# Kernel optimization log

Hardware: AMD Instinct MI355X
Metric: run time of the kernel (lower is better)

## Reference

```python
import jax, jax.numpy as jnp
import numpy as np

PI = float(np.pi)
BN_EPS = 1e-3
LN_EPS = 1e-5


def ssslu(x, shape, bias):
    # x * (sin(softsign(x) * shape*pi/2) + (bias + 1))
    s = x / (1.0 + jnp.abs(x))
    return x * (jnp.sin(s * (shape * PI / 2.0)) + (bias + 1.0))


def bn(x, g, b, m, v):
    inv = (g / jnp.sqrt(v + BN_EPS))[None, :, None, None]
    return (x - m[None, :, None, None]) * inv + b[None, :, None, None]


def conv2d(x, w, bias=None, pad=0):
    y = jax.lax.conv_general_dilated(x, w, (1, 1), [(pad, pad), (pad, pad)],
                                     dimension_numbers=('NCHW', 'OIHW', 'NCHW'))
    if bias is not None:
        y = y + bias[None, :, None, None]
    return y


def ln_silu(v):
    # LayerNorm (unit weight, zero bias) over last axis, then SiLU
    mu = jnp.mean(v, axis=-1, keepdims=True)
    var = jnp.mean(jnp.square(v - mu), axis=-1, keepdims=True)
    h = (v - mu) / jnp.sqrt(var + LN_EPS)
    return h * jax.nn.sigmoid(h)


def _forward(x, w_qkv, g_qkv, b_qkv, m_qkv, v_qkv,
             w_co, g_co, b_co, m_co, v_co,
             w_b1, bias_b1, g_b1, b_b1, m_b1, v_b1,
             w_b2, bias_b2, g_b2, b_b2, m_b2, v_b2):
    B, C, H, W = x.shape
    Q = (w_qkv.shape[0] - C) // 2
    # qkv Conv block: conv1x1 -> SSSLU(-3, 0.3) -> BN
    t = bn(ssslu(conv2d(x, w_qkv, pad=0), -3.0, 0.3), g_qkv, b_qkv, m_qkv, v_qkv)
    xq, xk, xv = jnp.split(t, [Q, 2 * Q], axis=1)
    # max-pooled Q/K rows and columns -> [B*Q, W] / [B*Q, H]
    qw = jnp.max(xq, axis=2).reshape(B * Q, W)
    kw = jnp.max(xk, axis=2).reshape(B * Q, W)
    qh = jnp.max(xq, axis=3).reshape(B * Q, H)
    kh = jnp.max(xk, axis=3).reshape(B * Q, H)
    # xaw[i,b] = max_a qw[i,a]*kw[i,b]; xah[i,a] = max_b qh[i,a]*kh[i,b]
    xaw = jnp.max(qw[:, :, None] * kw[:, None, :], axis=1)  # [BQ, W]
    xah = jnp.max(qh[:, :, None] * kh[:, None, :], axis=2)  # [BQ, H]
    xaw = ln_silu(xaw)
    xah = ln_silu(xah)
    xa = (xah[:, :, None] * xaw[:, None, :]).reshape(B, Q, H, W)
    # co: SSSLUConv(Q+C -> Q): conv3x3 -> BN -> SSSLU(1.0, 0)
    xa = jnp.concatenate([xa, xv], axis=1)
    xa = ssslu(bn(conv2d(xa, w_co, pad=1), g_co, b_co, m_co, v_co), 1.0, 0.0)
    # back[0]: Conv(Q -> C, k3, bias): conv -> SSSLU(-3, 0.3) -> BN
    xa = bn(ssslu(conv2d(xa, w_b1, bias_b1, pad=1), -3.0, 0.3), g_b1, b_b1, m_b1, v_b1)
    # back[1]: SSSLUConv(C -> C, k1, bias): conv -> BN -> SSSLU(0.8, 0)
    xa = ssslu(bn(conv2d(xa, w_b2, bias_b2, pad=0), g_b2, b_b2, m_b2, v_b2), 0.8, 0.0)
    # back[2]: Sigmoid; source returns the gate itself
    return jax.nn.sigmoid(xa)


def setup_inputs() -> dict:
    B, C, Q, H, W = 16, 256, 256, 64, 64
    key = jax.random.key(0)
    ks = jax.random.split(key, 32)

    def w_init(k, o, i, kh, kw):
        return jax.random.normal(k, (o, i, kh, kw), jnp.float32) * (1.0 / np.sqrt(i * kh * kw))

    def bn_params(k, c):
        k1, k2, k3, k4 = jax.random.split(k, 4)
        g = jax.random.uniform(k1, (c,), jnp.float32, 0.5, 1.5)
        b = jax.random.normal(k2, (c,), jnp.float32) * 0.1
        m = jax.random.normal(k3, (c,), jnp.float32) * 0.1
        v = jax.random.uniform(k4, (c,), jnp.float32, 0.5, 1.5)
        return g, b, m, v

    x = jax.random.normal(ks[0], (B, C, H, W), jnp.float32)
    w_qkv = w_init(ks[1], 2 * Q + C, C, 1, 1)
    g_qkv, b_qkv, m_qkv, v_qkv = bn_params(ks[2], 2 * Q + C)
    w_co = w_init(ks[3], Q, Q + C, 3, 3)
    g_co, b_co, m_co, v_co = bn_params(ks[4], Q)
    w_b1 = w_init(ks[5], C, Q, 3, 3)
    bias_b1 = jax.random.normal(ks[6], (C,), jnp.float32) * 0.05
    g_b1, b_b1, m_b1, v_b1 = bn_params(ks[7], C)
    w_b2 = w_init(ks[8], C, C, 1, 1)
    bias_b2 = jax.random.normal(ks[9], (C,), jnp.float32) * 0.05
    g_b2, b_b2, m_b2, v_b2 = bn_params(ks[10], C)
    return dict(x=x, w_qkv=w_qkv, g_qkv=g_qkv, b_qkv=b_qkv, m_qkv=m_qkv, v_qkv=v_qkv,
                w_co=w_co, g_co=g_co, b_co=b_co, m_co=m_co, v_co=v_co,
                w_b1=w_b1, bias_b1=bias_b1, g_b1=g_b1, b_b1=b_b1, m_b1=m_b1, v_b1=v_b1,
                w_b2=w_b2, bias_b2=bias_b2, g_b2=g_b2, b_b2=b_b2, m_b2=m_b2, v_b2=v_b2)


def reference(x, w_qkv, g_qkv, b_qkv, m_qkv, v_qkv,
              w_co, g_co, b_co, m_co, v_co,
              w_b1, bias_b1, g_b1, b_b1, m_b1, v_b1,
              w_b2, bias_b2, g_b2, b_b2, m_b2, v_b2):
    return _forward(x, w_qkv, g_qkv, b_qkv, m_qkv, v_qkv,
                    w_co, g_co, b_co, m_co, v_co,
                    w_b1, bias_b1, g_b1, b_b1, m_b1, v_b1,
                    w_b2, bias_b2, g_b2, b_b2, m_b2, v_b2)
```

## Files before the change

kernel.cpp:

```cpp
#include <hip/hip_runtime.h>
#include <hip/hip_bf16.h>
#include <math.h>

#define PI_F 3.14159265358979323846f

typedef unsigned short u16;
typedef unsigned int   u32;
typedef float    f32x4 __attribute__((ext_vector_type(4)));
typedef _Float16 f16x8 __attribute__((ext_vector_type(8)));
typedef u16      u16x8 __attribute__((ext_vector_type(8)));
typedef u16      u16x4 __attribute__((ext_vector_type(4)));

__device__ __forceinline__ u16 f2h(float f){ union{ _Float16 h; u16 u; } c; c.h = (_Float16)f; return c.u; }
__device__ __forceinline__ float h2f(u16 u){ union{ u16 u; _Float16 h; } c; c.u = u; return (float)c.h; }

__device__ __forceinline__ void gl16(const void* g, void* l){
  __builtin_amdgcn_global_load_lds((const __attribute__((address_space(1))) u32*)g,
                                   (__attribute__((address_space(3))) u32*)l, 16, 0, 0);
}

__device__ __forceinline__ int SWZ(int r){ return (r>>1)&3; }

__device__ __forceinline__ float wred_max(float v){
#pragma unroll
  for (int m = 32; m; m >>= 1) v = fmaxf(v, __shfl_xor(v, m));
  return v;
}
__device__ __forceinline__ float wred_min(float v){
#pragma unroll
  for (int m = 32; m; m >>= 1) v = fminf(v, __shfl_xor(v, m));
  return v;
}
__device__ __forceinline__ float wred_sum(float v){
#pragma unroll
  for (int m = 32; m; m >>= 1) v += __shfl_xor(v, m);
  return v;
}

__device__ __forceinline__ float ssslu_f(float x, float shp, float bp1){
  float s = x / (1.0f + fabsf(x));
  return x * (__sinf(s * shp) + bp1);
}

__device__ __forceinline__ float epi_val(float v, float4 p, float shp, float bp1, int ORDER, bool SIG){
  v += p.w;
  if (ORDER == 0){ v = ssslu_f(v, shp, bp1); v = (v - p.z) * p.x + p.y; }
  else           { v = (v - p.z) * p.x + p.y; v = ssslu_f(v, shp, bp1); }
  if (SIG) v = 1.f / (1.f + __expf(-v));
  return v;
}

__device__ __forceinline__ void atomicMaxF(float* a, float v){
  if (v >= 0.f) atomicMax(reinterpret_cast<int*>(a), __float_as_int(v));
  else          atomicMin(reinterpret_cast<unsigned int*>(a), __float_as_uint(v));
}

__device__ __forceinline__ f16x8 mul8h(u16x8 a, u16x8 b){
  union{ u16x8 u; f16x8 h; } A, B; A.u = a; B.u = b;
  return A.h * B.h;
}

__global__ __launch_bounds__(256)
void xpose_k(const float* __restrict__ X, u16* __restrict__ XH)
{
  __shared__ u16 L[16384];
  const int tid = threadIdx.x;
  const int b = blockIdx.x >> 6, h = blockIdx.x & 63;
  const float* xp = X + (size_t)b * 256 * 4096 + h * 64;
#pragma unroll
  for (int i = 0; i < 16; ++i){
    int ci = i * 16 + (tid >> 4);
    int w4 = (tid & 15) * 4;
    float4 v = *(const float4*)(xp + (size_t)ci * 4096 + w4);
    int sw = 4 * ((ci >> 3) & 15);
    u16x4 d;
    d[0] = f2h(v.x); d[1] = f2h(v.y); d[2] = f2h(v.z); d[3] = f2h(v.w);
    *(u16x4*)&L[ci * 64 + (w4 ^ sw)] = d;
  }
  __syncthreads();
  u16* out = XH + (((size_t)b * 4096 + (size_t)h * 64) << 8);
#pragma unroll
  for (int it = 0; it < 8; ++it){
    int w   = it * 8 + (tid >> 5);
    int m   = tid & 31;
    int ci0 = m * 8;
    int base = (w & ~3) ^ (4 * (m & 15));
    int wl   = w & 3;
    u16x8 o;
#pragma unroll
    for (int k = 0; k < 8; ++k)
      o[k] = L[(ci0 + k) * 64 + base + wl];
    *(u16x8*)&out[w * 256 + ci0] = o;
  }
}

template<int CI_T, bool CAT>
__global__ __launch_bounds__(512, 2)
void conv3_mfma(const u16* __restrict__ Apk, const u16* __restrict__ Bg,
                u16* __restrict__ DstH, const float4* __restrict__ pp,
                const u16* __restrict__ xahT_, const u16* __restrict__ xawT_,
                float shp, float bp1, int ORDER)
{
  constexpr int NCC = CI_T / 32;
  constexpr int NIT = NCC * 3;
  __shared__ __align__(16) u16 sAB[73728];

  const int tid  = threadIdx.x;
  const int lane = tid & 63;
  const int wv   = tid >> 6;
  const int wm   = wv >> 2;
  const int wn   = wv & 3;
  const int l15  = lane & 15, l4 = lane >> 4;

  const int bx  = blockIdx.x;
  const int bid = (bx & 7) * 32 + (bx >> 3);
  const int b   = bid >> 4;
  const int r0  = (bid & 15) * 4;

  auto STAGE = [&](int it2){
    int d2 = it2 % 3, c2 = it2 / 3;
    if (d2 == 0){
      int bufB = c2 & 1;
#pragma unroll
      for (int j = 0; j < 3; ++j){
        int rr  = 2 * j + (tid >> 8);
        int hh  = r0 - 1 + rr; hh = min(63, max(0, hh));
        int rem = tid & 255;
        int w   = rem >> 2, s = rem & 3;
        int ci0 = c2 * 32 + ((s ^ SWZ(w + 1)) << 3);
        if (CAT && c2 < 8){
          u16x8 vh = *(const u16x8*)&xahT_[((b * 64 + hh) << 8) + ci0];
          u16x8 vw = *(const u16x8*)&xawT_[((b * 64 + w ) << 8) + ci0];
          *(f16x8*)&sAB[49152 + bufB * 12288 + rr * 2048 + w * 32 + s * 8] = mul8h(vh, vw);
        } else {
          int ci = CAT ? (ci0 - 256) : ci0;
          const u16* src = Bg + (((size_t)b * 4096 + hh * 64 + w) << 8) + ci;
          gl16(src, &sAB[49152 + bufB * 12288 + rr * 2048 + (wv & 3) * 512]);
        }
      }
    }
    int bufA = it2 & 1;
#pragma unroll
    for (int j2 = 0; j2 < 3; ++j2){
      int tap = d2 * 3 + j2;
      const u16* base = Apk + (size_t)tap * 256 * CI_T + c2 * 32;
#pragma unroll
      for (int i = 0; i < 2; ++i){
        int row = i * 128 + (tid >> 2);
        int s   = tid & 3;
        const u16* src = base + (size_t)row * CI_T + ((s ^ SWZ(row)) << 3);
        gl16(src, &sAB[bufA * 24576 + j2 * 8192 + (i * 128 + wv * 16) * 32]);
      }
    }
  };

  f32x4 acc[8][4];
#pragma unroll
  for (int i = 0; i < 8; ++i)
#pragma unroll
    for (int j = 0; j < 4; ++j){ acc[i][j][0]=0.f; acc[i][j][1]=0.f; acc[i][j][2]=0.f; acc[i][j][3]=0.f; }

  STAGE(0);
  __syncthreads();

  for (int it = 0; it < NIT; ++it){
    if (it + 1 < NIT) STAGE(it + 1);

    const int d = it % 3, c = it / 3;
    const int bufA = it & 1, bufB = c & 1;
    const int brow = wn + d;
    const bool rowok = ((unsigned)(r0 + wn + d - 1)) < 64u;

#pragma unroll
    for (int dw = 0; dw < 3; ++dw){
      f16x8 afr[8], bfr[4];
#pragma unroll
      for (int fm = 0; fm < 8; ++fm){
        int m  = wm * 128 + fm * 16 + l15;
        int sl = l4 ^ SWZ(m);
        afr[fm] = *(const f16x8*)&sAB[bufA * 24576 + dw * 8192 + m * 32 + sl * 8];
      }
#pragma unroll
      for (int fn = 0; fn < 4; ++fn){
        int w_in = fn * 16 + l15 + dw - 1;
        int wc   = min(63, max(0, w_in));
        int sl2  = l4 ^ SWZ(wc + 1);
        f16x8 t  = *(const f16x8*)&sAB[49152 + bufB * 12288 + brow * 2048 + wc * 32 + sl2 * 8];
        bool ok  = rowok && (((unsigned)w_in) < 64u);
        bfr[fn]  = ok ? t : (f16x8)(_Float16)0;
      }
      __builtin_amdgcn_s_setprio(1);
#pragma unroll
      for (int fm = 0; fm < 8; ++fm)
#pragma unroll
        for (int fn = 0; fn < 4; ++fn)
          acc[fm][fn] = __builtin_amdgcn_mfma_f32_16x16x32_f16(afr[fm], bfr[fn], acc[fm][fn], 0, 0, 0);
      __builtin_amdgcn_s_setprio(0);
    }
    __syncthreads();
  }

  const int h = r0 + wn;
#pragma unroll
  for (int fm = 0; fm < 8; ++fm){
    const int cobase = wm * 128 + fm * 16 + 4 * l4;
    float4 P0 = pp[cobase], P1 = pp[cobase+1], P2 = pp[cobase+2], P3 = pp[cobase+3];
#pragma unroll
    for (int fn = 0; fn < 4; ++fn){
      int w = fn * 16 + l15;
      float v0 = epi_val(acc[fm][fn][0], P0, shp, bp1, ORDER, false);
      float v1 = epi_val(acc[fm][fn][1], P1, shp, bp1, ORDER, false);
      float v2 = epi_val(acc[fm][fn][2], P2, shp, bp1, ORDER, false);
      float v3 = epi_val(acc[fm][fn][3], P3, shp, bp1, ORDER, false);
      uint2 st;
      st.x = (u32)f2h(v0) | ((u32)f2h(v1) << 16);
      st.y = (u32)f2h(v2) | ((u32)f2h(v3) << 16);
      *(uint2*)&DstH[(((size_t)b * 4096 + (size_t)h * 64 + w) << 8) + cobase] = st;
    }
  }
}

template<int SRC, int EPI, int HLOOP>
__global__ __launch_bounds__(256)
void conv_mfma(const u16* __restrict__ Apk, const u16* __restrict__ Bg,
               u16* __restrict__ DstH, float* __restrict__ DstF,
               const float4* __restrict__ pp,
               const float* __restrict__ Xf,
               float* __restrict__ qwp, float* __restrict__ kwp,
               float* __restrict__ qhp, float* __restrict__ khp,
               float shp, float bp1, int ORDER, int M)
{
  constexpr int NCC = 8;
  constexpr int HG  = 64 / HLOOP;
  __shared__ __align__(16) u16 sA[2][8192];
  __shared__ __align__(16) u16 sB[2][2112];

  const int tid  = threadIdx.x;
  const int lane = tid & 63;
  const int wv   = tid >> 6;
  const int bx   = blockIdx.x;
  const int b    = bx / HG;
  const int h0   = (bx % HG) * HLOOP;
  const int m0   = blockIdx.y * 256;

  f32x4 acc[4][4];
  f32x4 cmax[4][4];
  if (EPI == 0){
#pragma unroll
    for (int i = 0; i < 4; ++i)
#pragma unroll
      for (int j = 0; j < 4; ++j){ cmax[i][j][0]=-3.0e38f; cmax[i][j][1]=-3.0e38f; cmax[i][j][2]=-3.0e38f; cmax[i][j][3]=-3.0e38f; }
  }

  for (int hi = 0; hi < HLOOP; ++hi){
    const int h = h0 + hi;
#pragma unroll
    for (int i = 0; i < 4; ++i)
#pragma unroll
      for (int j = 0; j < 4; ++j){ acc[i][j][0]=0.f; acc[i][j][1]=0.f; acc[i][j][2]=0.f; acc[i][j][3]=0.f; }

    auto stageA = [&](int c, int buf){
      const u16* base = Apk + (size_t)m0 * 256 + c * 32;
#pragma unroll
      for (int i = 0; i < 4; ++i){
        int row = i * 64 + (tid >> 2);
        int s   = tid & 3;
        const u16* src = base + (size_t)row * 256 + ((s ^ SWZ(row)) << 3);
        gl16(src, &sA[buf][(i * 64 + wv * 16) * 32]);
      }
    };
    auto stageB = [&](int c, int buf){
      const int w = tid >> 2, s = tid & 3, r = w + 1;
      if (SRC == 0){
        int ci0 = c * 32 + ((s ^ SWZ(r)) << 3);
        const float* xp = Xf + ((size_t)(b * 256 + ci0)) * 4096 + h * 64 + w;
        u16x8 v;
#pragma unroll
        for (int j = 0; j < 8; ++j) v[j] = f2h(xp[(size_t)j * 4096]);
        *(u16x8*)&sB[buf][r * 32 + s * 8] = v;
      } else {
        const u16* src = Bg + (((size_t)b * 4096 + h * 64 + w) << 8) + c * 32 + ((s ^ SWZ(r)) << 3);
        gl16(src, &sB[buf][(1 + wv * 16) * 32]);
      }
    };

    __syncthreads();
    stageA(0, 0);
    stageB(0, 0);
    __syncthreads();

    for (int it = 0; it < NCC; ++it){
      if (it + 1 < NCC){ stageA(it + 1, (it + 1) & 1); stageB(it + 1, (it + 1) & 1); }
      f16x8 afr[4], bfr[4];
#pragma unroll
      for (int fm = 0; fm < 4; ++fm){
        int row = wv * 64 + fm * 16 + (lane & 15);
        int sl  = (lane >> 4) ^ SWZ(row);
        afr[fm] = *(const f16x8*)&sA[it & 1][row * 32 + sl * 8];
      }
#pragma unroll
      for (int fn = 0; fn < 4; ++fn){
        int r  = fn * 16 + (lane & 15) + 1;
        int sl = (lane >> 4) ^ SWZ(r);
        bfr[fn] = *(const f16x8*)&sB[it & 1][r * 32 + sl * 8];
      }
      __builtin_amdgcn_s_setprio(1);
#pragma unroll
      for (int fm = 0; fm < 4; ++fm)
#pragma unroll
        for (int fn = 0; fn < 4; ++fn)
          acc[fm][fn] = __builtin_amdgcn_mfma_f32_16x16x32_f16(afr[fm], bfr[fn], acc[fm][fn], 0, 0, 0);
      __builtin_amdgcn_s_setprio(0);
      __syncthreads();
    }

    const int l15 = lane & 15, l4 = lane >> 4;
    if (EPI == 0){
#pragma unroll
      for (int fm = 0; fm < 4; ++fm){
        const int cobase = m0 + wv * 64 + fm * 16 + 4 * l4;
        float4 P0 = pp[cobase], P1 = pp[cobase+1], P2 = pp[cobase+2], P3 = pp[cobase+3];
        f32x4 ev[4];
#pragma unroll
        for (int fn = 0; fn < 4; ++fn){
          ev[fn][0] = epi_val(acc[fm][fn][0], P0, shp, bp1, ORDER, false);
          ev[fn][1] = epi_val(acc[fm][fn][1], P1, shp, bp1, ORDER, false);
          ev[fn][2] = epi_val(acc[fm][fn][2], P2, shp, bp1, ORDER, false);
          ev[fn][3] = epi_val(acc[fm][fn][3], P3, shp, bp1, ORDER, false);
#pragma unroll
          for (int r = 0; r < 4; ++r) cmax[fm][fn][r] = fmaxf(cmax[fm][fn][r], ev[fn][r]);
        }
#pragma unroll
        for (int r = 0; r < 4; ++r){
          float mv = fmaxf(fmaxf(ev[0][r], ev[1][r]), fmaxf(ev[2][r], ev[3][r]));
          mv = fmaxf(mv, __shfl_xor(mv, 1));
          mv = fmaxf(mv, __shfl_xor(mv, 2));
          mv = fmaxf(mv, __shfl_xor(mv, 4));
          mv = fmaxf(mv, __shfl_xor(mv, 8));
          if (l15 == 0){
            int q = (cobase + r) & 255;
            float* rowp = (m0 == 0) ? qhp : khp;
            rowp[(((b << 8) | q) << 6) + h] = mv;
          }
        }
      }
    } else if (EPI == 1){
#pragma unroll
      for (int fm = 0; fm < 4; ++fm){
        const int cobase = wv * 64 + fm * 16 + 4 * l4;
        float4 P0 = pp[cobase], P1 = pp[cobase+1], P2 = pp[cobase+2], P3 = pp[cobase+3];
#pragma unroll
        for (int fn = 0; fn < 4; ++fn){
          int w = fn * 16 + l15;
          float v0 = epi_val(acc[fm][fn][0], P0, shp, bp1, ORDER, false);
          float v1 = epi_val(acc[fm][fn][1], P1, shp, bp1, ORDER, false);
          float v2 = epi_val(acc[fm][fn][2], P2, shp, bp1, ORDER, false);
          float v3 = epi_val(acc[fm][fn][3], P3, shp, bp1, ORDER, false);
          uint2 st;
          st.x = (u32)f2h(v0) | ((u32)f2h(v1) << 16);
          st.y = (u32)f2h(v2) | ((u32)f2h(v3) << 16);
          *(uint2*)&DstH[(((size_t)b * 4096 + (size_t)h * 64 + w) << 8) + cobase] = st;
        }
      }
    } else {
#pragma unroll
      for (int fm = 0; fm < 4; ++fm){
        const int cobase = wv * 64 + fm * 16 + 4 * l4;
        float4 P0 = pp[cobase], P1 = pp[cobase+1], P2 = pp[cobase+2], P3 = pp[cobase+3];
#pragma unroll
        for (int fn = 0; fn < 4; ++fn){
          int w = fn * 16 + l15;
          float v0 = epi_val(acc[fm][fn][0], P0, shp, bp1, ORDER, true);
          float v1 = epi_val(acc[fm][fn][1], P1, shp, bp1, ORDER, true);
          float v2 = epi_val(acc[fm][fn][2], P2, shp, bp1, ORDER, true);
          float v3 = epi_val(acc[fm][fn][3], P3, shp, bp1, ORDER, true);
          size_t base = ((size_t)(b * 256 + cobase)) * 4096 + h * 64 + w;
          DstF[base]          = v0;
          DstF[base + 4096]   = v1;
          DstF[base + 2*4096] = v2;
          DstF[base + 3*4096] = v3;
        }
      }
    }
  }

  if (EPI == 0){
    const int l15 = lane & 15, l4 = lane >> 4;
    float* colp = (m0 == 0) ? qwp : kwp;
#pragma unroll
    for (int fm = 0; fm < 4; ++fm)
#pragma unroll
      for (int fn = 0; fn < 4; ++fn)
#pragma unroll
        for (int r = 0; r < 4; ++r){
          int q = (m0 + wv * 64 + fm * 16 + 4 * l4 + r) & 255;
          int w = fn * 16 + l15;
          atomicMaxF(&colp[(((b << 8) | q) << 6) + w], cmax[fm][fn][r]);
        }
  }
}

__device__ __forceinline__ float ln_silu_wave(float v){
  float mu = wred_sum(v) * (1.f / 64.f);
  float d = v - mu;
  float var = wred_sum(d * d) * (1.f / 64.f);
  float hn = d * rsqrtf(var + 1e-5f);
  return hn / (1.f + __expf(-hn));
}

__global__ void attn_k(const float* __restrict__ qw, const float* __restrict__ kw,
                       const float* __restrict__ qh, const float* __restrict__ kh,
                       u16* __restrict__ xahT, u16* __restrict__ xawT)
{
  int row  = blockIdx.x * 4 + (threadIdx.x >> 6);
  int lane = threadIdx.x & 63;
  int idx  = (row << 6) + lane;
  float qwv = qw[idx], kwv = kw[idx], qhv = qh[idx], khv = kh[idx];
  float Pq = wred_max(qwv), mq = wred_min(qwv);
  float Pk = wred_max(khv), mk = wred_min(khv);
  float aw = fmaxf(kwv * Pq, kwv * mq);
  float ah = fmaxf(qhv * Pk, qhv * mk);
  aw = ln_silu_wave(aw);
  ah = ln_silu_wave(ah);
  int b = row >> 8, q = row & 255;
  xawT[((b * 64 + lane) << 8) + q] = f2h(aw);
  xahT[((b * 64 + lane) << 8) + q] = f2h(ah);
}

__global__ void pack_k(const float* __restrict__ wqkv, const float* __restrict__ wco,
                       const float* __restrict__ wb1, const float* __restrict__ wb2,
                       const float* gq, const float* bq, const float* mq, const float* vq,
                       const float* gc, const float* bc, const float* mc, const float* vc,
                       const float* g1, const float* b1, const float* m1, const float* v1, const float* bias1,
                       const float* g2, const float* b2, const float* m2, const float* v2, const float* bias2,
                       u16* __restrict__ WQ, u16* __restrict__ WCO, u16* __restrict__ WB1, u16* __restrict__ WB2,
                       float4* __restrict__ PP)
{
  const int E0 = 196608, E1 = 196608 + 1179648, E2 = 196608 + 1179648 + 589824, E3 = 2031616;
  int i = blockIdx.x * 256 + threadIdx.x;
  if (i >= E3 + 1536) return;
  if (i < E0){ WQ[i] = f2h(wqkv[i]); }
  else if (i < E1){
    int d = i - E0; int tap = d / 131072; int rm = d % 131072; int m = rm >> 9; int ci = rm & 511;
    WCO[d] = f2h(wco[(size_t)((m << 9) | ci) * 9 + tap]);
  } else if (i < E2){
    int d = i - E1; int tap = d / 65536; int rm = d & 65535; int m = rm >> 8; int ci = rm & 255;
    WB1[d] = f2h(wb1[(size_t)((m << 8) | ci) * 9 + tap]);
  } else if (i < E3){
    int d = i - E2; WB2[d] = f2h(wb2[d]);
  } else {
    int c = i - E3;
    float g, be, mm, vv, bi;
    if (c < 768){ g = gq[c]; be = bq[c]; mm = mq[c]; vv = vq[c]; bi = 0.f; }
    else if (c < 1024){ int j = c - 768;  g = gc[j]; be = bc[j]; mm = mc[j]; vv = vc[j]; bi = 0.f; }
    else if (c < 1280){ int j = c - 1024; g = g1[j]; be = b1[j]; mm = m1[j]; vv = v1[j]; bi = bias1[j]; }
    else              { int j = c - 1280; g = g2[j]; be = b2[j]; mm = m2[j]; vv = v2[j]; bi = bias2[j]; }
    PP[c] = make_float4(g / sqrtf(vv + 1e-3f), be, mm, bi);
  }
}

__global__ void initpool_k(float* __restrict__ p)
{
  int i = blockIdx.x * 1024 + threadIdx.x * 4;
  float4 v = make_float4(-3.0e38f, -3.0e38f, -3.0e38f, -3.0e38f);
  *(float4*)(p + i) = v;
}

extern "C" void kernel_launch(void* const* d_in, const int* in_sizes, int n_in,
                              void* d_out, int out_size, void* d_ws, size_t ws_size,
                              hipStream_t stream)
{
  const float* x       = (const float*)d_in[0];
  const float* w_qkv   = (const float*)d_in[1];
  const float* g_qkv   = (const float*)d_in[2];
  const float* b_qkv   = (const float*)d_in[3];
  const float* m_qkv   = (const float*)d_in[4];
  const float* v_qkv   = (const float*)d_in[5];
  const float* w_co    = (const float*)d_in[6];
  const float* g_co    = (const float*)d_in[7];
  const float* b_co    = (const float*)d_in[8];
  const float* m_co    = (const float*)d_in[9];
  const float* v_co    = (const float*)d_in[10];
  const float* w_b1    = (const float*)d_in[11];
  const float* bias_b1 = (const float*)d_in[12];
  const float* g_b1    = (const float*)d_in[13];
  const float* b_b1    = (const float*)d_in[14];
  const float* m_b1    = (const float*)d_in[15];
  const float* v_b1    = (const float*)d_in[16];
  const float* w_b2    = (const float*)d_in[17];
  const float* bias_b2 = (const float*)d_in[18];
  const float* g_b2    = (const float*)d_in[19];
  const float* b_b2    = (const float*)d_in[20];
  const float* m_b2    = (const float*)d_in[21];
  const float* v_b2    = (const float*)d_in[22];
  float* out = (float*)d_out;

  char* W = (char*)d_ws;
  u16*    WQ   = (u16*)(W + 0);
  u16*    WCO  = (u16*)(W + 393216);
  u16*    WB1  = (u16*)(W + 2752512);
  u16*    WB2  = (u16*)(W + 3932160);
  float4* PP   = (float4*)(W + 4063232);
  u16*    TV   = (u16*)(W + 4087808);
  u16*    XAHT = (u16*)(W + 37642240);
  u16*    XAWT = (u16*)(W + 38166528);
  u16*    XH   = (u16*)(W + 38690816);
  u16*    Y1   = (u16*)(W + 38690816);
  u16*    Y2   = TV;
  float*  qw_  = (float*)(W + 72245248);
  float*  kw_  = (float*)(W + 73293824);
  float*  qh_  = (float*)(W + 74342400);
  float*  kh_  = (float*)(W + 75390976);

  const size_t NEED = 76439552;
  if (ws_size < NEED) return;

  const float SHP_N3 = -3.0f * PI_F * 0.5f;
  const float SHP_1  =  1.0f * PI_F * 0.5f;
  const float SHP_08 =  0.8f * PI_F * 0.5f;

  dim3 blk(256);

  pack_k<<<7942, blk, 0, stream>>>(w_qkv, w_co, w_b1, w_b2,
      g_qkv, b_qkv, m_qkv, v_qkv,
      g_co,  b_co,  m_co,  v_co,
      g_b1,  b_b1,  m_b1,  v_b1,  bias_b1,
      g_b2,  b_b2,  m_b2,  v_b2,  bias_b2,
      WQ, WCO, WB1, WB2, PP);

  initpool_k<<<512, blk, 0, stream>>>(qw_);

  xpose_k<<<1024, blk, 0, stream>>>(x, XH);

  conv_mfma<1, 0, 4><<<dim3(256, 2), blk, 0, stream>>>(
      WQ, XH, nullptr, nullptr, PP, nullptr,
      qw_, kw_, qh_, kh_, SHP_N3, 1.3f, 0, 512);

  conv_mfma<1, 1, 1><<<dim3(1024, 1), blk, 0, stream>>>(
      WQ + (size_t)512 * 256, XH, TV, nullptr, PP + 512, nullptr,
      nullptr, nullptr, nullptr, nullptr, SHP_N3, 1.3f, 0, 256);

  attn_k<<<1024, blk, 0, stream>>>(qw_, kw_, qh_, kh_, XAHT, XAWT);

  conv3_mfma<512, true><<<256, 512, 0, stream>>>(
      WCO, TV, Y1, PP + 768, XAHT, XAWT, SHP_1, 1.0f, 1);

  conv3_mfma<256, false><<<256, 512, 0, stream>>>(
      WB1, Y1, Y2, PP + 1024, nullptr, nullptr, SHP_N3, 1.3f, 0);

  conv_mfma<1, 2, 1><<<dim3(1024, 1), blk, 0, stream>>>(
      WB2, Y2, nullptr, out, PP + 1280, nullptr,
      nullptr, nullptr, nullptr, nullptr, SHP_08, 1.0f, 1, 256);
}
```

Before: 452.9 us.

## Use larger 256x256-tile 512-thread kernel for V-projection and final 1x1 convs

```diff
diff --git a/kernel.cpp b/kernel.cpp
--- a/kernel.cpp
+++ b/kernel.cpp
@@ -220,6 +220,109 @@
   }
 }
 
+template<int EPI>
+__global__ __launch_bounds__(512, 2)
+void conv1_big(const u16* __restrict__ Apk, const u16* __restrict__ Bg,
+               u16* __restrict__ DstH, float* __restrict__ DstF,
+               const float4* __restrict__ pp,
+               float shp, float bp1, int ORDER)
+{
+  __shared__ __align__(16) u16 sA[2][8192];
+  __shared__ __align__(16) u16 sB[2][8192];
+
+  const int tid  = threadIdx.x;
+  const int lane = tid & 63;
+  const int wv   = tid >> 6;
+  const int wm   = wv >> 2;
+  const int wn   = wv & 3;
+  const int l15  = lane & 15, l4 = lane >> 4;
+
+  const int bx  = blockIdx.x;
+  const int bid = (bx & 7) * 32 + (bx >> 3);
+  const int b   = bid >> 4;
+  const int h0  = (bid & 15) * 4;
+
+  auto STAGE = [&](int c){
+    int buf = c & 1;
+#pragma unroll
+    for (int j = 0; j < 2; ++j){
+      int g = j * 512 + tid;
+      int m = g >> 2, s = g & 3;
+      const u16* srcA = Apk + (size_t)m * 256 + c * 32 + ((s ^ SWZ(m)) << 3);
+      gl16(srcA, &sA[buf][(j * 512 + wv * 64) * 8]);
+      int r = g >> 8, w = (g >> 2) & 63;
+      const u16* srcB = Bg + (((size_t)b * 4096 + (h0 + r) * 64 + w) << 8) + c * 32 + ((s ^ SWZ(w)) << 3);
+      gl16(srcB, &sB[buf][(j * 512 + wv * 64) * 8]);
+    }
+  };
+
+  f32x4 acc[8][4];
+#pragma unroll
+  for (int i = 0; i < 8; ++i)
+#pragma unroll
+    for (int j = 0; j < 4; ++j){ acc[i][j][0]=0.f; acc[i][j][1]=0.f; acc[i][j][2]=0.f; acc[i][j][3]=0.f; }
+
+  STAGE(0);
+  __syncthreads();
+
+  for (int c = 0; c < 8; ++c){
+    if (c + 1 < 8) STAGE(c + 1);
+    const int buf = c & 1;
+    f16x8 afr[8], bfr[4];
+#pragma unroll
+    for (int fm = 0; fm < 8; ++fm){
+      int m  = wm * 128 + fm * 16 + l15;
+      int sl = l4 ^ SWZ(m);
+      afr[fm] = *(const f16x8*)&sA[buf][m * 32 + sl * 8];
+    }
+#pragma unroll
+    for (int fn = 0; fn < 4; ++fn){
+      int w  = fn * 16 + l15;
+      int sl = l4 ^ SWZ(w);
+      bfr[fn] = *(const f16x8*)&sB[buf][(wn * 64 + w) * 32 + sl * 8];
+    }
+    __builtin_amdgcn_s_setprio(1);
+#pragma unroll
+    for (int fm = 0; fm < 8; ++fm)
+#pragma unroll
+      for (int fn = 0; fn < 4; ++fn)
+        acc[fm][fn] = __builtin_amdgcn_mfma_f32_16x16x32_f16(afr[fm], bfr[fn], acc[fm][fn], 0, 0, 0);
+    __builtin_amdgcn_s_setprio(0);
+    __syncthreads();
+  }
+
+  const int h = h0 + wn;
+#pragma unroll
+  for (int fm = 0; fm < 8; ++fm){
+    const int cobase = wm * 128 + fm * 16 + 4 * l4;
+    float4 P0 = pp[cobase], P1 = pp[cobase+1], P2 = pp[cobase+2], P3 = pp[cobase+3];
+#pragma unroll
+    for (int fn = 0; fn < 4; ++fn){
+      int w = fn * 16 + l15;
+      if (EPI == 1){
+        float v0 = epi_val(acc[fm][fn][0], P0, shp, bp1, ORDER, false);
+        float v1 = epi_val(acc[fm][fn][1], P1, shp, bp1, ORDER, false);
+        float v2 = epi_val(acc[fm][fn][2], P2, shp, bp1, ORDER, false);
+        float v3 = epi_val(acc[fm][fn][3], P3, shp, bp1, ORDER, false);
+        uint2 st;
+        st.x = (u32)f2h(v0) | ((u32)f2h(v1) << 16);
+        st.y = (u32)f2h(v2) | ((u32)f2h(v3) << 16);
+        *(uint2*)&DstH[(((size_t)b * 4096 + (size_t)h * 64 + w) << 8) + cobase] = st;
+      } else {
+        float v0 = epi_val(acc[fm][fn][0], P0, shp, bp1, ORDER, true);
+        float v1 = epi_val(acc[fm][fn][1], P1, shp, bp1, ORDER, true);
+        float v2 = epi_val(acc[fm][fn][2], P2, shp, bp1, ORDER, true);
+        float v3 = epi_val(acc[fm][fn][3], P3, shp, bp1, ORDER, true);
+        size_t base = ((size_t)(b * 256 + cobase)) * 4096 + (size_t)h * 64 + w;
+        DstF[base]          = v0;
+        DstF[base + 4096]   = v1;
+        DstF[base + 2*4096] = v2;
+        DstF[base + 3*4096] = v3;
+      }
+    }
+  }
+}
+
 template<int SRC, int EPI, int HLOOP>
 __global__ __launch_bounds__(256)
 void conv_mfma(const u16* __restrict__ Apk, const u16* __restrict__ Bg,
@@ -342,43 +445,6 @@
             float* rowp = (m0 == 0) ? qhp : khp;
             rowp[(((b << 8) | q) << 6) + h] = mv;
           }
-        }
-      }
-    } else if (EPI == 1){
-#pragma unroll
-      for (int fm = 0; fm < 4; ++fm){
-        const int cobase = wv * 64 + fm * 16 + 4 * l4;
-        float4 P0 = pp[cobase], P1 = pp[cobase+1], P2 = pp[cobase+2], P3 = pp[cobase+3];
-#pragma unroll
-        for (int fn = 0; fn < 4; ++fn){
-          int w = fn * 16 + l15;
-          float v0 = epi_val(acc[fm][fn][0], P0, shp, bp1, ORDER, false);
-          float v1 = epi_val(acc[fm][fn][1], P1, shp, bp1, ORDER, false);
-          float v2 = epi_val(acc[fm][fn][2], P2, shp, bp1, ORDER, false);
-          float v3 = epi_val(acc[fm][fn][3], P3, shp, bp1, ORDER, false);
-          uint2 st;
-          st.x = (u32)f2h(v0) | ((u32)f2h(v1) << 16);
-          st.y = (u32)f2h(v2) | ((u32)f2h(v3) << 16);
-          *(uint2*)&DstH[(((size_t)b * 4096 + (size_t)h * 64 + w) << 8) + cobase] = st;
-        }
-      }
-    } else {
-#pragma unroll
-      for (int fm = 0; fm < 4; ++fm){
-        const int cobase = wv * 64 + fm * 16 + 4 * l4;
-        float4 P0 = pp[cobase], P1 = pp[cobase+1], P2 = pp[cobase+2], P3 = pp[cobase+3];
-#pragma unroll
-        for (int fn = 0; fn < 4; ++fn){
-          int w = fn * 16 + l15;
-          float v0 = epi_val(acc[fm][fn][0], P0, shp, bp1, ORDER, true);
-          float v1 = epi_val(acc[fm][fn][1], P1, shp, bp1, ORDER, true);
-          float v2 = epi_val(acc[fm][fn][2], P2, shp, bp1, ORDER, true);
-          float v3 = epi_val(acc[fm][fn][3], P3, shp, bp1, ORDER, true);
-          size_t base = ((size_t)(b * 256 + cobase)) * 4096 + h * 64 + w;
-          DstF[base]          = v0;
-          DstF[base + 4096]   = v1;
-          DstF[base + 2*4096] = v2;
-          DstF[base + 3*4096] = v3;
         }
       }
     }
@@ -536,9 +602,8 @@
       WQ, XH, nullptr, nullptr, PP, nullptr,
       qw_, kw_, qh_, kh_, SHP_N3, 1.3f, 0, 512);
 
-  conv_mfma<1, 1, 1><<<dim3(1024, 1), blk, 0, stream>>>(
-      WQ + (size_t)512 * 256, XH, TV, nullptr, PP + 512, nullptr,
-      nullptr, nullptr, nullptr, nullptr, SHP_N3, 1.3f, 0, 256);
+  conv1_big<1><<<256, 512, 0, stream>>>(
+      WQ + (size_t)512 * 256, XH, TV, nullptr, PP + 512, SHP_N3, 1.3f, 0);
 
   attn_k<<<1024, blk, 0, stream>>>(qw_, kw_, qh_, kh_, XAHT, XAWT);
 
@@ -548,7 +613,6 @@
   conv3_mfma<256, false><<<256, 512, 0, stream>>>(
       WB1, Y1, Y2, PP + 1024, nullptr, nullptr, SHP_N3, 1.3f, 0);
 
-  conv_mfma<1, 2, 1><<<dim3(1024, 1), blk, 0, stream>>>(
-      WB2, Y2, nullptr, out, PP + 1280, nullptr,
-      nullptr, nullptr, nullptr, nullptr, SHP_08, 1.0f, 1, 256);
-}
+  conv1_big<2><<<256, 512, 0, stream>>>(
+      WB2, Y2, nullptr, out, PP + 1280, SHP_08, 1.0f, 1);
+}
```

After: 447.8 us. No clear change (-1.1%).
